# Kernel optimization log

Hardware: AMD Instinct MI355X
Metric: run time of the kernel (lower is better)

## Reference

```python
import jax, jax.numpy as jnp
import numpy as np

N = 50000
E = 800000
IN_C = 128
HID = 64
OUT_C = 64
NUM_CLASSES = 10
H1 = 2
H2 = 1
NEG_SLOPE = 0.2  # PyG GATv2Conv default


def setup_inputs() -> dict:
    key = jax.random.key(0)
    ks = jax.random.split(key, 12)
    s = 0.05
    inp = {
        "x": jax.random.normal(ks[0], (N, IN_C), jnp.float32),
        "edge_index": jax.random.randint(ks[1], (2, E), 0, N, jnp.int64),
        "batch": jnp.zeros((N,), jnp.int64),
        # conv1 params (GATv2: separate lin_l / lin_r, att vector, output bias)
        "Wl1": jax.random.normal(ks[2], (H1 * HID, IN_C), jnp.float32) * s,
        "bl1": jnp.zeros((H1 * HID,), jnp.float32),
        "Wr1": jax.random.normal(ks[3], (H1 * HID, IN_C), jnp.float32) * s,
        "br1": jnp.zeros((H1 * HID,), jnp.float32),
        "att1": jax.random.normal(ks[4], (H1, HID), jnp.float32) * s,
        "bias1": jnp.zeros((H1 * HID,), jnp.float32),
        # conv2 params
        "Wl2": jax.random.normal(ks[5], (H2 * OUT_C, H1 * HID), jnp.float32) * s,
        "bl2": jnp.zeros((H2 * OUT_C,), jnp.float32),
        "Wr2": jax.random.normal(ks[6], (H2 * OUT_C, H1 * HID), jnp.float32) * s,
        "br2": jnp.zeros((H2 * OUT_C,), jnp.float32),
        "att2": jax.random.normal(ks[7], (H2, OUT_C), jnp.float32) * s,
        "bias2": jnp.zeros((OUT_C,), jnp.float32),
        # classifier head
        "Wc": jax.random.normal(ks[8], (NUM_CLASSES, OUT_C), jnp.float32) * s,
        "bc": jnp.zeros((NUM_CLASSES,), jnp.float32),
    }
    return inp


def _gatv2_conv(x, src, dst, Wl, bl, Wr, br, att, bias, heads, ch, concat):
    n = x.shape[0]
    xl = (x @ Wl.T + bl).reshape(n, heads, ch)  # messages from source
    xr = (x @ Wr.T + br).reshape(n, heads, ch)  # target-side transform
    e = xl[src] + xr[dst]                        # [Etot, H, C]
    e = jnp.where(e > 0, e, NEG_SLOPE * e)       # LeakyReLU
    score = jnp.einsum('ehc,hc->eh', e, att)     # [Etot, H]
    # segment softmax over incoming edges of each dst node
    m = jax.ops.segment_max(score, dst, num_segments=n)  # [N, H]
    m = jnp.where(jnp.isfinite(m), m, 0.0)
    ex = jnp.exp(score - m[dst])
    denom = jax.ops.segment_sum(ex, dst, num_segments=n)  # [N, H]
    alpha = ex / denom[dst]
    out = jax.ops.segment_sum(alpha[:, :, None] * xl[src], dst, num_segments=n)  # [N,H,C]
    if concat:
        out = out.reshape(n, heads * ch)
    else:
        out = out.mean(axis=1)
    return out + bias


def reference(x, edge_index, batch, Wl1, bl1, Wr1, br1, att1, bias1,
              Wl2, bl2, Wr2, br2, att2, bias2, Wc, bc):
    n = x.shape[0]
    # PyG GATv2Conv adds self-loops by default
    loops = jnp.arange(n, dtype=edge_index.dtype)
    src = jnp.concatenate([edge_index[0], loops])
    dst = jnp.concatenate([edge_index[1], loops])

    h = _gatv2_conv(x, src, dst, Wl1, bl1, Wr1, br1, att1, bias1, H1, HID, True)
    h = jax.nn.elu(h)  # dropout p=0 / eval -> identity
    h = _gatv2_conv(h, src, dst, Wl2, bl2, Wr2, br2, att2, bias2, H2, OUT_C, False)
    h = jax.nn.elu(h)
    logits = h @ Wc.T + bc  # [N, num_classes]
    return logits
```

## Files before the change

kernel.cpp:

```cpp
#include <hip/hip_runtime.h>
#include <hip/hip_bf16.h>

#define N_NODES 50000
#define E_EDGES 800000
#define NCLS 10
#define SCAN_BLOCKS 196

typedef short bfrag __attribute__((ext_vector_type(8)));
typedef float f32x4 __attribute__((ext_vector_type(4)));

__device__ __forceinline__ int rfl(int v) { return __builtin_amdgcn_readfirstlane(v); }

__device__ __forceinline__ unsigned short bf16rne(float x) {
    unsigned u = __float_as_uint(x);
    unsigned r = u + 0x7FFFu + ((u >> 16) & 1u);
    return (unsigned short)(r >> 16);
}

template <int CTRL, int RM>
__device__ __forceinline__ float dppadd(float x) {
    int s = __builtin_amdgcn_update_dpp(0, __float_as_int(x), CTRL, RM, 0xf, true);
    return x + __int_as_float(s);
}
__device__ __forceinline__ float rl63(float x) {
    return __int_as_float(__builtin_amdgcn_readlane(__float_as_int(x), 63));
}
__device__ __forceinline__ float rl31(float x) {
    return __int_as_float(__builtin_amdgcn_readlane(__float_as_int(x), 31));
}
__device__ __forceinline__ void dred1(float& x0) {
    x0 = dppadd<0x111, 0xf>(x0);
    x0 = dppadd<0x112, 0xf>(x0);
    x0 = dppadd<0x114, 0xf>(x0);
    x0 = dppadd<0x118, 0xf>(x0);
    x0 = dppadd<0x142, 0xa>(x0);
    x0 = dppadd<0x143, 0xc>(x0);
}
__device__ __forceinline__ void dred4(float& x0, float& x1, float& x2, float& x3) {
    x0 = dppadd<0x111, 0xf>(x0); x1 = dppadd<0x111, 0xf>(x1);
    x2 = dppadd<0x111, 0xf>(x2); x3 = dppadd<0x111, 0xf>(x3);
    x0 = dppadd<0x112, 0xf>(x0); x1 = dppadd<0x112, 0xf>(x1);
    x2 = dppadd<0x112, 0xf>(x2); x3 = dppadd<0x112, 0xf>(x3);
    x0 = dppadd<0x114, 0xf>(x0); x1 = dppadd<0x114, 0xf>(x1);
    x2 = dppadd<0x114, 0xf>(x2); x3 = dppadd<0x114, 0xf>(x3);
    x0 = dppadd<0x118, 0xf>(x0); x1 = dppadd<0x118, 0xf>(x1);
    x2 = dppadd<0x118, 0xf>(x2); x3 = dppadd<0x118, 0xf>(x3);
    x0 = dppadd<0x142, 0xa>(x0); x1 = dppadd<0x142, 0xa>(x1);
    x2 = dppadd<0x142, 0xa>(x2); x3 = dppadd<0x142, 0xa>(x3);
    x0 = dppadd<0x143, 0xc>(x0); x1 = dppadd<0x143, 0xc>(x1);
    x2 = dppadd<0x143, 0xc>(x2); x3 = dppadd<0x143, 0xc>(x3);
}
__device__ __forceinline__ void dredH(float& x) {
    x = dppadd<0x111, 0xf>(x);
    x = dppadd<0x112, 0xf>(x);
    x = dppadd<0x114, 0xf>(x);
    x = dppadd<0x118, 0xf>(x);
    x = dppadd<0x142, 0xa>(x);
}
__device__ __forceinline__ void dredH2(float& x, float& y) {
    x = dppadd<0x111, 0xf>(x); y = dppadd<0x111, 0xf>(y);
    x = dppadd<0x112, 0xf>(x); y = dppadd<0x112, 0xf>(y);
    x = dppadd<0x114, 0xf>(x); y = dppadd<0x114, 0xf>(y);
    x = dppadd<0x118, 0xf>(x); y = dppadd<0x118, 0xf>(y);
    x = dppadd<0x142, 0xa>(x); y = dppadd<0x142, 0xa>(y);
}
__device__ __forceinline__ float lrelu(float u) { return u > 0.f ? u : 0.2f * u; }
__device__ __forceinline__ float escore(float2 v, float2 xr2, float2 av) {
    float ux = v.x + xr2.x, uy = v.y + xr2.y;
    ux = fmaxf(ux, 0.2f * ux);
    uy = fmaxf(uy, 0.2f * uy);
    return ux * av.x + uy * av.y;
}

__global__ void k_count(const int* __restrict__ dst, int* __restrict__ deg) {
    int i = blockIdx.x * blockDim.x + threadIdx.x;
    if (i < E_EDGES) {
        unsigned d = (unsigned)dst[i];
        if (d < N_NODES) atomicAdd(&deg[d], 1);
    }
}

__global__ void k_scanA(const int* __restrict__ deg, int* __restrict__ incl,
                        int* __restrict__ bsum) {
    __shared__ int s[256];
    int i = blockIdx.x * 256 + threadIdx.x;
    int v = (i < N_NODES) ? deg[i] : 0;
    s[threadIdx.x] = v;
    __syncthreads();
    for (int off = 1; off < 256; off <<= 1) {
        int t = (threadIdx.x >= off) ? s[threadIdx.x - off] : 0;
        __syncthreads();
        s[threadIdx.x] += t;
        __syncthreads();
    }
    if (i < N_NODES) incl[i] = s[threadIdx.x];
    if (threadIdx.x == 255) bsum[blockIdx.x] = s[255];
}

__global__ void k_scanB(int* __restrict__ bsum) {
    __shared__ int s[256];
    int t = threadIdx.x;
    s[t] = (t < SCAN_BLOCKS) ? bsum[t] : 0;
    __syncthreads();
    for (int off = 1; off < 256; off <<= 1) {
        int v = (t >= off) ? s[t - off] : 0;
        __syncthreads();
        s[t] += v;
        __syncthreads();
    }
    if (t < SCAN_BLOCKS) bsum[t] = s[t];
}

__global__ void k_scanC(int* __restrict__ degcur, const int* __restrict__ incl,
                        const int* __restrict__ bsum, int* __restrict__ rowptr) {
    int i = blockIdx.x * 256 + threadIdx.x;
    if (i >= N_NODES) return;
    int base = (blockIdx.x == 0) ? 0 : bsum[blockIdx.x - 1];
    int d = degcur[i];
    int excl = base + incl[i] - d;
    rowptr[i] = excl;
    degcur[i] = excl;
    if (i == N_NODES - 1) rowptr[N_NODES] = base + incl[i];
}

__global__ void k_scatter(const int* __restrict__ src, const int* __restrict__ dst,
                          int* __restrict__ cursor, int* __restrict__ csr_src) {
    int i = blockIdx.x * blockDim.x + threadIdx.x;
    if (i < E_EDGES) {
        unsigned d = (unsigned)dst[i];
        if (d < N_NODES) {
            int p = atomicAdd(&cursor[d], 1);
            unsigned s = (unsigned)src[i];
            csr_src[p] = (s < N_NODES) ? (int)s : 0;
        }
    }
}

__global__ void k_splitW(const float* __restrict__ W, int n,
                         short* __restrict__ hi, short* __restrict__ lo) {
    int i = blockIdx.x * 256 + threadIdx.x;
    if (i < n) {
        float x = W[i];
        unsigned short h = bf16rne(x);
        float hf = __uint_as_float((unsigned)h << 16);
        unsigned short l = bf16rne(x - hf);
        hi[i] = (short)h;
        lo[i] = (short)l;
    }
}

template <int NCT>
__global__ __launch_bounds__(256) void k_mgemm(const float* __restrict__ X,
                                               const short* __restrict__ whl,
                                               const short* __restrict__ wll,
                                               const short* __restrict__ whr,
                                               const short* __restrict__ wlr,
                                               const float* __restrict__ bl,
                                               const float* __restrict__ br,
                                               float* __restrict__ Yl,
                                               float* __restrict__ Yr, int nrows) {
    const int NOUT = NCT * 16;
    int tid = threadIdx.x;
    int wv = tid >> 6, lane = tid & 63;
    int m = lane & 15, g = lane >> 4;
    int row = blockIdx.x * 64 + wv * 16 + m;
    int rowc = min(row, nrows - 1);

    bfrag ahi[4], alo[4];
    const float* xp = X + (size_t)rowc * 128 + g * 8;
#pragma unroll
    for (int kb = 0; kb < 4; ++kb) {
        float4 u0 = *(const float4*)(xp + kb * 32);
        float4 u1 = *(const float4*)(xp + kb * 32 + 4);
        float xs[8] = {u0.x, u0.y, u0.z, u0.w, u1.x, u1.y, u1.z, u1.w};
#pragma unroll
        for (int j = 0; j < 8; ++j) {
            unsigned short h = bf16rne(xs[j]);
            float hf = __uint_as_float((unsigned)h << 16);
            unsigned short l = bf16rne(xs[j] - hf);
            ahi[kb][j] = (short)h;
            alo[kb][j] = (short)l;
        }
    }

    f32x4 accl[NCT], accr[NCT];
#pragma unroll
    for (int ct = 0; ct < NCT; ++ct) {
        accl[ct] = (f32x4){0.f, 0.f, 0.f, 0.f};
        accr[ct] = (f32x4){0.f, 0.f, 0.f, 0.f};
    }

#pragma unroll
    for (int kb = 0; kb < 4; ++kb) {
#pragma unroll
        for (int ct = 0; ct < NCT; ++ct) {
            size_t wo = (size_t)(ct * 16 + m) * 128 + kb * 32 + g * 8;
            bfrag bhl = *(const bfrag*)(whl + wo);
            bfrag bll = *(const bfrag*)(wll + wo);
            bfrag bhr = *(const bfrag*)(whr + wo);
            bfrag blr = *(const bfrag*)(wlr + wo);
            accl[ct] = __builtin_amdgcn_mfma_f32_16x16x32_bf16(ahi[kb], bhl, accl[ct], 0, 0, 0);
            accl[ct] = __builtin_amdgcn_mfma_f32_16x16x32_bf16(alo[kb], bhl, accl[ct], 0, 0, 0);
            accl[ct] = __builtin_amdgcn_mfma_f32_16x16x32_bf16(ahi[kb], bll, accl[ct], 0, 0, 0);
            accr[ct] = __builtin_amdgcn_mfma_f32_16x16x32_bf16(ahi[kb], bhr, accr[ct], 0, 0, 0);
            accr[ct] = __builtin_amdgcn_mfma_f32_16x16x32_bf16(alo[kb], bhr, accr[ct], 0, 0, 0);
            accr[ct] = __builtin_amdgcn_mfma_f32_16x16x32_bf16(ahi[kb], blr, accr[ct], 0, 0, 0);
        }
    }

    int orow0 = blockIdx.x * 64 + wv * 16 + g * 4;
#pragma unroll
    for (int ct = 0; ct < NCT; ++ct) {
        int col = ct * 16 + m;
        float blv = bl[col], brv = br[col];
#pragma unroll
        for (int i = 0; i < 4; ++i) {
            int orow = orow0 + i;
            if (orow < nrows) {
                Yl[(size_t)orow * NOUT + col] = accl[ct][i] + blv;
                Yr[(size_t)orow * NOUT + col] = accr[ct][i] + brv;
            }
        }
    }
}

__global__ __launch_bounds__(256) void k_gat1(const float* __restrict__ xl,
                                              const float* __restrict__ xr,
                                              const int* __restrict__ rowptr,
                                              const int* __restrict__ csr,
                                              const float* __restrict__ att,
                                              const float* __restrict__ bias,
                                              float* __restrict__ out) {
    int node = blockIdx.x * 4 + (threadIdx.x >> 6);
    if (node >= N_NODES) return;
    node = rfl(node);
    int lane = threadIdx.x & 63;
    bool lo = lane < 32;
    const float2* xl2 = (const float2*)xl;
    size_t nb = (size_t)node * 64;
    float2 av = ((const float2*)att)[lane];
    float2 xr2 = ((const float2*)xr)[nb + lane];
    float2 sl2 = xl2[nb + lane];

    float p = escore(sl2, xr2, av);
    dredH(p);
    float e0 = __expf(rl31(p)), e1 = __expf(rl63(p));
    float ev = lo ? e0 : e1;
    float den = ev;
    float2 acc;
    acc.x = ev * sl2.x;
    acc.y = ev * sl2.y;

    int beg = rfl(rowptr[node]), end = rfl(rowptr[node + 1]);
    int cnt = end - beg;
    int np = cnt >> 1;
    if (np > 0) {
        const int* cp = csr + beg;
        int i0 = rfl(cp[0]), i1 = rfl(cp[1]);
        float2 A = xl2[(size_t)(unsigned)i0 * 64 + lane];
        float2 B = xl2[(size_t)(unsigned)i1 * 64 + lane];
        for (int q = 1; q <= np; ++q) {
            float2 nA = {0.f, 0.f}, nB = {0.f, 0.f};
            if (q < np) {
                int j0 = rfl(cp[2 * q]), j1 = rfl(cp[2 * q + 1]);
                nA = xl2[(size_t)(unsigned)j0 * 64 + lane];
                nB = xl2[(size_t)(unsigned)j1 * 64 + lane];
            }
            float pa = escore(A, xr2, av);
            float pb = escore(B, xr2, av);
            dredH2(pa, pb);
            float ea0 = __expf(rl31(pa)), ea1 = __expf(rl63(pa));
            float eb0 = __expf(rl31(pb)), eb1 = __expf(rl63(pb));
            float eva = lo ? ea0 : ea1;
            float evb = lo ? eb0 : eb1;
            den += eva + evb;
            acc.x = fmaf(eva, A.x, fmaf(evb, B.x, acc.x));
            acc.y = fmaf(eva, A.y, fmaf(evb, B.y, acc.y));
            A = nA; B = nB;
        }
    }
    if (cnt & 1) {
        int j = rfl(csr[end - 1]);
        float2 C = xl2[(size_t)(unsigned)j * 64 + lane];
        float pc = escore(C, xr2, av);
        dredH(pc);
        float ec0 = __expf(rl31(pc)), ec1 = __expf(rl63(pc));
        float evc = lo ? ec0 : ec1;
        den += evc;
        acc.x = fmaf(evc, C.x, acc.x);
        acc.y = fmaf(evc, C.y, acc.y);
    }
    float2 b2 = ((const float2*)bias)[lane];
    float ox = acc.x / den + b2.x;
    float oy = acc.y / den + b2.y;
    ox = ox > 0.f ? ox : expm1f(ox);
    oy = oy > 0.f ? oy : expm1f(oy);
    float2 o2 = {ox, oy};
    ((float2*)out)[nb + lane] = o2;
}

__global__ __launch_bounds__(256) void k_gat2(const float* __restrict__ xl,
                                              const float* __restrict__ xr,
                                              const int* __restrict__ rowptr,
                                              const int* __restrict__ csr,
                                              const float* __restrict__ att,
                                              const float* __restrict__ bias,
                                              float* __restrict__ out) {
    int node = blockIdx.x * 4 + (threadIdx.x >> 6);
    if (node >= N_NODES) return;
    node = rfl(node);
    int lane = threadIdx.x & 63;
    float a = att[lane];
    size_t nb = (size_t)node << 6;
    float xrv = xr[nb + lane];
    float slv = xl[nb + lane];
    float p = lrelu(slv + xrv) * a;
    dred1(p);
    float w = __expf(rl63(p));
    float den = w;
    float acc = w * slv;

    int beg = rfl(rowptr[node]), end = rfl(rowptr[node + 1]);
    int cnt = end - beg;
    int quads = cnt >> 2;
    if (quads > 0) {
        const int* cp = csr + beg;
        int i0 = rfl(cp[0]), i1 = rfl(cp[1]), i2 = rfl(cp[2]), i3 = rfl(cp[3]);
        float A = (xl + ((size_t)(unsigned)i0 << 6))[lane];
        float B = (xl + ((size_t)(unsigned)i1 << 6))[lane];
        float C = (xl + ((size_t)(unsigned)i2 << 6))[lane];
        float D = (xl + ((size_t)(unsigned)i3 << 6))[lane];
        for (int q = 1; q <= quads; ++q) {
            float nA = 0.f, nB = 0.f, nC = 0.f, nD = 0.f;
            if (q < quads) {
                int j0 = rfl(cp[4 * q]), j1 = rfl(cp[4 * q + 1]);
                int j2 = rfl(cp[4 * q + 2]), j3 = rfl(cp[4 * q + 3]);
                nA = (xl + ((size_t)(unsigned)j0 << 6))[lane];
                nB = (xl + ((size_t)(unsigned)j1 << 6))[lane];
                nC = (xl + ((size_t)(unsigned)j2 << 6))[lane];
                nD = (xl + ((size_t)(unsigned)j3 << 6))[lane];
            }
            float pa = lrelu(A + xrv) * a;
            float pb = lrelu(B + xrv) * a;
            float pc = lrelu(C + xrv) * a;
            float pd = lrelu(D + xrv) * a;
            dred4(pa, pb, pc, pd);
            float ea = __expf(rl63(pa)), eb = __expf(rl63(pb));
            float ec = __expf(rl63(pc)), ed = __expf(rl63(pd));
            den += (ea + eb) + (ec + ed);
            acc = fmaf(ea, A, fmaf(eb, B, fmaf(ec, C, fmaf(ed, D, acc))));
            A = nA; B = nB; C = nC; D = nD;
        }
    }
    int rem = cnt & 3;
    if (rem) {
        int j0 = rfl(csr[end - rem]);
        int j1 = (rem > 1) ? rfl(csr[end - rem + 1]) : j0;
        int j2 = (rem > 2) ? rfl(csr[end - rem + 2]) : j0;
        float A = (xl + ((size_t)(unsigned)j0 << 6))[lane];
        float B = (xl + ((size_t)(unsigned)j1 << 6))[lane];
        float C = (xl + ((size_t)(unsigned)j2 << 6))[lane];
        float pa = lrelu(A + xrv) * a;
        float pb = lrelu(B + xrv) * a;
        float pc = lrelu(C + xrv) * a;
        float pd = 0.f;
        dred4(pa, pb, pc, pd);
        float ea = __expf(rl63(pa));
        float eb = (rem > 1) ? __expf(rl63(pb)) : 0.f;
        float ec = (rem > 2) ? __expf(rl63(pc)) : 0.f;
        den += ea + eb + ec;
        acc = fmaf(ea, A, fmaf(eb, B, fmaf(ec, C, acc)));
    }
    float o = acc / den + bias[lane];
    out[nb + lane] = o > 0.f ? o : expm1f(o);
}

__global__ __launch_bounds__(256) void k_head(const float* __restrict__ H,
                                              const float* __restrict__ Wc,
                                              const float* __restrict__ bc,
                                              float* __restrict__ out) {
    __shared__ float Ws[NCLS * 64];
    __shared__ float bs[NCLS];
    for (int i = threadIdx.x; i < NCLS * 64; i += 256) Ws[i] = Wc[i];
    if (threadIdx.x < NCLS) bs[threadIdx.x] = bc[threadIdx.x];
    __syncthreads();
    int n = blockIdx.x * 256 + threadIdx.x;
    if (n >= N_NODES) return;
    const float4* hp = (const float4*)(H + (size_t)n * 64);
    float acc[NCLS] = {};
#pragma unroll
    for (int k4 = 0; k4 < 16; ++k4) {
        float4 hv = hp[k4];
#pragma unroll
        for (int c = 0; c < NCLS; ++c) {
            acc[c] = fmaf(hv.x, Ws[c * 64 + k4 * 4 + 0], acc[c]);
            acc[c] = fmaf(hv.y, Ws[c * 64 + k4 * 4 + 1], acc[c]);
            acc[c] = fmaf(hv.z, Ws[c * 64 + k4 * 4 + 2], acc[c]);
            acc[c] = fmaf(hv.w, Ws[c * 64 + k4 * 4 + 3], acc[c]);
        }
    }
#pragma unroll
    for (int c = 0; c < NCLS; ++c) out[(size_t)n * NCLS + c] = acc[c] + bs[c];
}

extern "C" void kernel_launch(void* const* d_in, const int* in_sizes, int n_in,
                              void* d_out, int out_size, void* d_ws, size_t ws_size,
                              hipStream_t stream) {
    const float* x     = (const float*)d_in[0];
    const int*   ei    = (const int*)d_in[1];
    const int*   srcp  = ei;
    const int*   dstp  = ei + E_EDGES;
    const float* Wl1   = (const float*)d_in[3];
    const float* bl1   = (const float*)d_in[4];
    const float* Wr1   = (const float*)d_in[5];
    const float* br1   = (const float*)d_in[6];
    const float* att1  = (const float*)d_in[7];
    const float* bias1 = (const float*)d_in[8];
    const float* Wl2   = (const float*)d_in[9];
    const float* bl2   = (const float*)d_in[10];
    const float* Wr2   = (const float*)d_in[11];
    const float* br2   = (const float*)d_in[12];
    const float* att2  = (const float*)d_in[13];
    const float* bias2 = (const float*)d_in[14];
    const float* Wc    = (const float*)d_in[15];
    const float* bc    = (const float*)d_in[16];

    float* fA = (float*)d_ws;
    float* fB = fA + (size_t)N_NODES * 128;
    float* fC = fB + (size_t)N_NODES * 128;
    int* rowptr = (int*)(fC + (size_t)N_NODES * 128);
    int* degcur = rowptr + (N_NODES + 1);
    int* csr    = degcur + N_NODES;
    size_t woff = ((size_t)(csr + E_EDGES) - (size_t)d_ws + 15) & ~(size_t)15;
    short* whiL = (short*)((char*)d_ws + woff);
    short* wloL = whiL + 16384;
    short* whiR = wloL + 16384;
    short* wloR = whiR + 16384;
    int* incl = (int*)(wloR + 16384);
    int* bsum = incl + N_NODES;

    hipMemsetAsync(degcur, 0, N_NODES * sizeof(int), stream);
    k_count<<<(E_EDGES + 255) / 256, 256, 0, stream>>>(dstp, degcur);
    k_scanA<<<SCAN_BLOCKS, 256, 0, stream>>>(degcur, incl, bsum);
    k_scanB<<<1, 256, 0, stream>>>(bsum);
    k_scanC<<<SCAN_BLOCKS, 256, 0, stream>>>(degcur, incl, bsum, rowptr);
    k_scatter<<<(E_EDGES + 255) / 256, 256, 0, stream>>>(srcp, dstp, degcur, csr);

    int gblocks = (N_NODES + 63) / 64;

    k_splitW<<<64, 256, 0, stream>>>(Wl1, 16384, whiL, wloL);
    k_splitW<<<64, 256, 0, stream>>>(Wr1, 16384, whiR, wloR);
    k_mgemm<8><<<gblocks, 256, 0, stream>>>(x, whiL, wloL, whiR, wloR, bl1, br1, fA, fB, N_NODES);
    k_gat1<<<(N_NODES + 3) / 4, 256, 0, stream>>>(fA, fB, rowptr, csr, att1, bias1, fC);

    k_splitW<<<32, 256, 0, stream>>>(Wl2, 8192, whiL, wloL);
    k_splitW<<<32, 256, 0, stream>>>(Wr2, 8192, whiR, wloR);
    k_mgemm<4><<<gblocks, 256, 0, stream>>>(fC, whiL, wloL, whiR, wloR, bl2, br2, fA, fB, N_NODES);
    k_gat2<<<(N_NODES + 3) / 4, 256, 0, stream>>>(fA, fB, rowptr, csr, att2, bias2, fC);

    k_head<<<(N_NODES + 255) / 256, 256, 0, stream>>>(fC, Wc, bc, (float*)d_out);
}
```

Baseline: 425.2 us.

## Split fused left/right projection GEMM into separate column-tiled launches

The combined kernel that computed both lin_l and lin_r projections with up to 16 accumulator tiles per wave is replaced by a single-output kernel with 4 column tiles per wave. Column blocks are spread over a second grid dimension, and separate launches handle the left and right weights. This lowers register pressure and raises occupancy and parallelism. In exchange, the input X is read and split into bf16 hi/lo several times (four times for layer 1, twice for layer 2), and there are more kernel launches.

```diff
diff --git a/kernel.cpp b/kernel.cpp
--- a/kernel.cpp
+++ b/kernel.cpp
@@ -149,20 +149,17 @@
     }
 }
 
-template <int NCT>
-__global__ __launch_bounds__(256) void k_mgemm(const float* __restrict__ X,
-                                               const short* __restrict__ whl,
-                                               const short* __restrict__ wll,
-                                               const short* __restrict__ whr,
-                                               const short* __restrict__ wlr,
-                                               const float* __restrict__ bl,
-                                               const float* __restrict__ br,
-                                               float* __restrict__ Yl,
-                                               float* __restrict__ Yr, int nrows) {
-    const int NOUT = NCT * 16;
+template <int NOUT>
+__global__ __launch_bounds__(256) void k_mgemmS(const float* __restrict__ X,
+                                                const short* __restrict__ whi,
+                                                const short* __restrict__ wlo,
+                                                const float* __restrict__ b,
+                                                float* __restrict__ Y, int nrows) {
+    const int NCT = 4;
     int tid = threadIdx.x;
     int wv = tid >> 6, lane = tid & 63;
     int m = lane & 15, g = lane >> 4;
+    int colbase = blockIdx.y * 64;
     int row = blockIdx.x * 64 + wv * 16 + m;
     int rowc = min(row, nrows - 1);
 
@@ -183,43 +180,32 @@
         }
     }
 
-    f32x4 accl[NCT], accr[NCT];
+    f32x4 acc[NCT];
+#pragma unroll
+    for (int ct = 0; ct < NCT; ++ct) acc[ct] = (f32x4){0.f, 0.f, 0.f, 0.f};
+
+#pragma unroll
+    for (int kb = 0; kb < 4; ++kb) {
+#pragma unroll
+        for (int ct = 0; ct < NCT; ++ct) {
+            size_t wo = (size_t)(colbase + ct * 16 + m) * 128 + kb * 32 + g * 8;
+            bfrag bh = *(const bfrag*)(whi + wo);
+            bfrag bl_ = *(const bfrag*)(wlo + wo);
+            acc[ct] = __builtin_amdgcn_mfma_f32_16x16x32_bf16(ahi[kb], bh, acc[ct], 0, 0, 0);
+            acc[ct] = __builtin_amdgcn_mfma_f32_16x16x32_bf16(alo[kb], bh, acc[ct], 0, 0, 0);
+            acc[ct] = __builtin_amdgcn_mfma_f32_16x16x32_bf16(ahi[kb], bl_, acc[ct], 0, 0, 0);
+        }
+    }
+
+    int orow0 = blockIdx.x * 64 + wv * 16 + g * 4;
 #pragma unroll
     for (int ct = 0; ct < NCT; ++ct) {
-        accl[ct] = (f32x4){0.f, 0.f, 0.f, 0.f};
-        accr[ct] = (f32x4){0.f, 0.f, 0.f, 0.f};
-    }
-
-#pragma unroll
-    for (int kb = 0; kb < 4; ++kb) {
-#pragma unroll
-        for (int ct = 0; ct < NCT; ++ct) {
-            size_t wo = (size_t)(ct * 16 + m) * 128 + kb * 32 + g * 8;
-            bfrag bhl = *(const bfrag*)(whl + wo);
-            bfrag bll = *(const bfrag*)(wll + wo);
-            bfrag bhr = *(const bfrag*)(whr + wo);
-            bfrag blr = *(const bfrag*)(wlr + wo);
-            accl[ct] = __builtin_amdgcn_mfma_f32_16x16x32_bf16(ahi[kb], bhl, accl[ct], 0, 0, 0);
-            accl[ct] = __builtin_amdgcn_mfma_f32_16x16x32_bf16(alo[kb], bhl, accl[ct], 0, 0, 0);
-            accl[ct] = __builtin_amdgcn_mfma_f32_16x16x32_bf16(ahi[kb], bll, accl[ct], 0, 0, 0);
-            accr[ct] = __builtin_amdgcn_mfma_f32_16x16x32_bf16(ahi[kb], bhr, accr[ct], 0, 0, 0);
-            accr[ct] = __builtin_amdgcn_mfma_f32_16x16x32_bf16(alo[kb], bhr, accr[ct], 0, 0, 0);
-            accr[ct] = __builtin_amdgcn_mfma_f32_16x16x32_bf16(ahi[kb], blr, accr[ct], 0, 0, 0);
-        }
-    }
-
-    int orow0 = blockIdx.x * 64 + wv * 16 + g * 4;
-#pragma unroll
-    for (int ct = 0; ct < NCT; ++ct) {
-        int col = ct * 16 + m;
-        float blv = bl[col], brv = br[col];
+        int col = colbase + ct * 16 + m;
+        float bv = b[col];
 #pragma unroll
         for (int i = 0; i < 4; ++i) {
             int orow = orow0 + i;
-            if (orow < nrows) {
-                Yl[(size_t)orow * NOUT + col] = accl[ct][i] + blv;
-                Yr[(size_t)orow * NOUT + col] = accr[ct][i] + brv;
-            }
+            if (orow < nrows) Y[(size_t)orow * NOUT + col] = acc[ct][i] + bv;
         }
     }
 }
@@ -450,12 +436,16 @@
 
     k_splitW<<<64, 256, 0, stream>>>(Wl1, 16384, whiL, wloL);
     k_splitW<<<64, 256, 0, stream>>>(Wr1, 16384, whiR, wloR);
-    k_mgemm<8><<<gblocks, 256, 0, stream>>>(x, whiL, wloL, whiR, wloR, bl1, br1, fA, fB, N_NODES);
+    dim3 g1(gblocks, 2);
+    k_mgemmS<128><<<g1, 256, 0, stream>>>(x, whiL, wloL, bl1, fA, N_NODES);
+    k_mgemmS<128><<<g1, 256, 0, stream>>>(x, whiR, wloR, br1, fB, N_NODES);
     k_gat1<<<(N_NODES + 3) / 4, 256, 0, stream>>>(fA, fB, rowptr, csr, att1, bias1, fC);
 
     k_splitW<<<32, 256, 0, stream>>>(Wl2, 8192, whiL, wloL);
     k_splitW<<<32, 256, 0, stream>>>(Wr2, 8192, whiR, wloR);
-    k_mgemm<4><<<gblocks, 256, 0, stream>>>(fC, whiL, wloL, whiR, wloR, bl2, br2, fA, fB, N_NODES);
+    dim3 g2(gblocks, 1);
+    k_mgemmS<64><<<g2, 256, 0, stream>>>(fC, whiL, wloL, bl2, fA, N_NODES);
+    k_mgemmS<64><<<g2, 256, 0, stream>>>(fC, whiR, wloR, br2, fB, N_NODES);
     k_gat2<<<(N_NODES + 3) / 4, 256, 0, stream>>>(fA, fB, rowptr, csr, att2, bias2, fC);
 
     k_head<<<(N_NODES + 255) / 256, 256, 0, stream>>>(fC, Wc, bc, (float*)d_out);
```

Measured after the change: 429.5 us. About the same (+1.0%).
